# Optimization experiments

Hardware: AMD Instinct MI355X
Metric: run time of the kernel (lower is better)

## Reference

```python
import jax, jax.numpy as jnp
import numpy as np

N = 50000  # total nodes


def sage_conv(x, src, dst, Wl, Wr, b):
    # PyG SAGEConv with mean aggregation: out = mean_{j in N(i)} x_j @ Wl + x_i @ Wr + b
    agg = jax.ops.segment_sum(x[src], dst, num_segments=N)
    deg = jax.ops.segment_sum(jnp.ones((src.shape[0],), x.dtype), dst, num_segments=N)
    mean = agg / jnp.maximum(deg, 1.0)[:, None]
    return mean @ Wl + x @ Wr + b


def setup_inputs() -> dict:
    key = jax.random.key(0)
    ks = jax.random.split(key, 16)
    F_in, D, H, B, E1, E2, A = 128, 64, 128, 16, 800000, 200000, 2000
    s = lambda fan: 1.0 / np.sqrt(fan)
    return {
        "x": jax.random.normal(ks[0], (N, F_in), jnp.float32),
        "edge_index": jax.random.randint(ks[1], (2, E1), 0, N),
        "new_edges": jax.random.randint(ks[2], (B, 2, E2), 0, N),
        "target_nodes": jax.random.randint(ks[3], (B,), 0, N),
        "regions": jax.random.randint(ks[4], (B, A), 0, N),
        "W1l": jax.random.normal(ks[5], (F_in, D), jnp.float32) * s(F_in),
        "W1r": jax.random.normal(ks[6], (F_in, D), jnp.float32) * s(F_in),
        "b1": jnp.zeros((D,), jnp.float32),
        "W2l": jax.random.normal(ks[7], (D, D), jnp.float32) * s(D),
        "W2r": jax.random.normal(ks[8], (D, D), jnp.float32) * s(D),
        "b2": jnp.zeros((D,), jnp.float32),
        "Wm": jax.random.normal(ks[9], (D, H), jnp.float32) * s(D),
        "bm": jnp.zeros((H,), jnp.float32),
        "Wo": jax.random.normal(ks[10], (H, D), jnp.float32) * s(H),
        "bo": jnp.zeros((D,), jnp.float32),
    }


def reference(x, edge_index, new_edges, target_nodes, regions,
              W1l, W1r, b1, W2l, W2r, b2, Wm, bm, Wo, bo):
    # shared conv1 over base graph
    h1 = jax.nn.relu(sage_conv(x, edge_index[0], edge_index[1], W1l, W1r, b1))  # [N,D]

    def per_graph(edges, t, region):
        h2 = jax.nn.relu(sage_conv(h1, edges[0], edges[1], W2l, W2r, b2))  # [N,D]
        target_embed = h2[t]          # [D]
        region_embed = h2[region]     # [A,D]
        e = jax.nn.relu(region_embed @ Wm + bm)  # [A,H]
        r = e @ Wo + bo                           # [A,D]
        return r @ target_embed                   # [A]  (bilin_q)

    q = jax.vmap(per_graph)(new_edges, target_nodes, regions)  # [B,A]
    return q
```

## Files before the change

### kernel.cpp

```cpp
#include <hip/hip_runtime.h>
#include <hip/hip_bf16.h>

#define NN 50000
#define E1C 800000
#define E2C 200000
#define BC 16
#define AC 2000
#define FIN 128
#define DD 64
#define HH 128
#define SLOTS (AC + 1)
#define SCAP 64
#define SCAP2 32
#define NPART 8
#define PSZ (NN / NPART)
#define DEGB 2048
#define MARKB ((BC * SLOTS + 255) / 256)
#define GH1B ((NN + 3) / 4)
#define FILTB 196
#define Q_NBLK 32

__device__ __forceinline__ unsigned short f2bf(float f) {
  unsigned int u = __float_as_uint(f);
  unsigned int r = (u + 0x7FFFu + ((u >> 16) & 1u)) >> 16;
  return (unsigned short)r;
}
__device__ __forceinline__ float bf2f(unsigned short h) {
  return __uint_as_float((unsigned int)h << 16);
}

__global__ __launch_bounds__(256, 2) void k_lin1(const float* __restrict__ x,
    const float* __restrict__ W1l, const float* __restrict__ W1r,
    const float* __restrict__ b1,
    unsigned short* __restrict__ y, float* __restrict__ z) {
  __shared__ __align__(16) float Wsh[FIN][FIN];
  for (int i = threadIdx.x; i < FIN * FIN; i += 256) {
    int k = i >> 7, c = i & 127;
    Wsh[k][c] = (c < DD) ? W1l[k * DD + c] : W1r[k * DD + (c - DD)];
  }
  const int cg = threadIdx.x & 31, c0 = cg * 4;
  const int rg = threadIdx.x >> 5, r0 = rg * 4;
  float4 bias = make_float4(0.f, 0.f, 0.f, 0.f);
  if (cg >= 16) bias = *(const float4*)(b1 + c0 - DD);
  __syncthreads();
  const int ntiles = (NN + 31) / 32;
  for (int t = blockIdx.x; t < ntiles; t += gridDim.x) {
    int base = t * 32;
    int gr0 = base + r0;
    const float* xp0 = x + (size_t)min(gr0 + 0, NN - 1) * FIN;
    const float* xp1 = x + (size_t)min(gr0 + 1, NN - 1) * FIN;
    const float* xp2 = x + (size_t)min(gr0 + 2, NN - 1) * FIN;
    const float* xp3 = x + (size_t)min(gr0 + 3, NN - 1) * FIN;
    float acc[4][4] = {};
#pragma unroll 4
    for (int kk = 0; kk < FIN; kk += 4) {
      float4 xq0 = *(const float4*)(xp0 + kk);
      float4 xq1 = *(const float4*)(xp1 + kk);
      float4 xq2 = *(const float4*)(xp2 + kk);
      float4 xq3 = *(const float4*)(xp3 + kk);
#pragma unroll
      for (int j = 0; j < 4; ++j) {
        float4 wv = *(const float4*)&Wsh[kk + j][c0];
        float x0 = (j == 0) ? xq0.x : (j == 1) ? xq0.y : (j == 2) ? xq0.z : xq0.w;
        float x1 = (j == 0) ? xq1.x : (j == 1) ? xq1.y : (j == 2) ? xq1.z : xq1.w;
        float x2 = (j == 0) ? xq2.x : (j == 1) ? xq2.y : (j == 2) ? xq2.z : xq2.w;
        float x3 = (j == 0) ? xq3.x : (j == 1) ? xq3.y : (j == 2) ? xq3.z : xq3.w;
        acc[0][0] = fmaf(x0, wv.x, acc[0][0]); acc[0][1] = fmaf(x0, wv.y, acc[0][1]);
        acc[0][2] = fmaf(x0, wv.z, acc[0][2]); acc[0][3] = fmaf(x0, wv.w, acc[0][3]);
        acc[1][0] = fmaf(x1, wv.x, acc[1][0]); acc[1][1] = fmaf(x1, wv.y, acc[1][1]);
        acc[1][2] = fmaf(x1, wv.z, acc[1][2]); acc[1][3] = fmaf(x1, wv.w, acc[1][3]);
        acc[2][0] = fmaf(x2, wv.x, acc[2][0]); acc[2][1] = fmaf(x2, wv.y, acc[2][1]);
        acc[2][2] = fmaf(x2, wv.z, acc[2][2]); acc[2][3] = fmaf(x2, wv.w, acc[2][3]);
        acc[3][0] = fmaf(x3, wv.x, acc[3][0]); acc[3][1] = fmaf(x3, wv.y, acc[3][1]);
        acc[3][2] = fmaf(x3, wv.z, acc[3][2]); acc[3][3] = fmaf(x3, wv.w, acc[3][3]);
      }
    }
#pragma unroll
    for (int i = 0; i < 4; ++i) {
      int gr = base + r0 + i;
      if (gr < NN) {
        if (cg < 16) {
          ushort4 ob = make_ushort4(f2bf(acc[i][0]), f2bf(acc[i][1]),
                                    f2bf(acc[i][2]), f2bf(acc[i][3]));
          *(ushort4*)(y + (size_t)gr * DD + c0) = ob;
        } else {
          float4 o = make_float4(acc[i][0] + bias.x, acc[i][1] + bias.y,
                                 acc[i][2] + bias.z, acc[i][3] + bias.w);
          *(float4*)(z + (size_t)gr * DD + (c0 - DD)) = o;
        }
      }
    }
  }
}

__global__ __launch_bounds__(256) void k_prep(const int* __restrict__ src,
    const int* __restrict__ dst, int* __restrict__ degi, int* __restrict__ slots,
    const int* __restrict__ regions, const int* __restrict__ targets,
    int* __restrict__ mark, int* __restrict__ rep) {
  if (blockIdx.x < DEGB) {
    int part = blockIdx.x & (NPART - 1);
    int lb   = blockIdx.x >> 3;
    int nlb  = DEGB >> 3;
    int lo = part * PSZ, hi = lo + PSZ;
    for (int e = lb * 256 + threadIdx.x; e < E1C; e += nlb * 256) {
      int d = dst[e];
      if (d >= lo && d < hi) {
        int p = atomicAdd(&degi[d], 1);
        if (p < SCAP) slots[(size_t)d * SCAP + p] = src[e];
      }
    }
  } else {
    int i = (blockIdx.x - DEGB) * 256 + threadIdx.x;
    if (i >= BC * SLOTS) return;
    int b = i / SLOTS, k = i % SLOTS;
    int node = (k < AC) ? regions[b * AC + k] : targets[b];
    int old = atomicCAS(&mark[b * NN + node], -1, k);
    rep[i] = (old < 0) ? k : old;
  }
}

__global__ __launch_bounds__(256) void k_sparse2(const int* __restrict__ degi,
    const int* __restrict__ slots, const unsigned short* __restrict__ y,
    const float* __restrict__ z, float* __restrict__ h1,
    const int* __restrict__ ne, const int* __restrict__ mark,
    int* __restrict__ deg2i, int* __restrict__ slots2) {
  if (blockIdx.x < GH1B) {
    int w = blockIdx.x * 4 + (threadIdx.x >> 6);
    int lane = threadIdx.x & 63;
    if (w >= NN) return;
    int deg = degi[w];
    int n = min(deg, SCAP);
    const int* sp = slots + (size_t)w * SCAP;
    float acc = 0.f;
    int j = 0;
    for (; j + 4 <= n; j += 4) {
      int s0 = sp[j], s1 = sp[j + 1], s2 = sp[j + 2], s3 = sp[j + 3];
      float a0 = bf2f(y[(size_t)s0 * DD + lane]);
      float a1 = bf2f(y[(size_t)s1 * DD + lane]);
      float a2 = bf2f(y[(size_t)s2 * DD + lane]);
      float a3 = bf2f(y[(size_t)s3 * DD + lane]);
      acc += (a0 + a1) + (a2 + a3);
    }
    for (; j < n; ++j) acc += bf2f(y[(size_t)sp[j] * DD + lane]);
    float m = acc / fmaxf((float)deg, 1.f);
    h1[(size_t)w * DD + lane] = fmaxf(m + z[(size_t)w * DD + lane], 0.f);
  } else {
    int fid = blockIdx.x - GH1B;
    int b = fid / FILTB, eb = fid % FILTB;
    int e = eb * 1024 + threadIdx.x * 4;
    if (e >= E2C) return;
    const int* srcp = ne + (size_t)b * 2 * E2C;
    const int* dstp = srcp + E2C;
    int4 d4 = *(const int4*)(dstp + e);
    const int* mb = mark + (size_t)b * NN;
    int k0 = mb[d4.x], k1 = mb[d4.y], k2 = mb[d4.z], k3 = mb[d4.w];
    if (k0 >= 0) { int p = atomicAdd(&deg2i[b * SLOTS + k0], 1);
      if (p < SCAP2) slots2[((size_t)b * SLOTS + k0) * SCAP2 + p] = srcp[e]; }
    if (k1 >= 0) { int p = atomicAdd(&deg2i[b * SLOTS + k1], 1);
      if (p < SCAP2) slots2[((size_t)b * SLOTS + k1) * SCAP2 + p] = srcp[e + 1]; }
    if (k2 >= 0) { int p = atomicAdd(&deg2i[b * SLOTS + k2], 1);
      if (p < SCAP2) slots2[((size_t)b * SLOTS + k2) * SCAP2 + p] = srcp[e + 2]; }
    if (k3 >= 0) { int p = atomicAdd(&deg2i[b * SLOTS + k3], 1);
      if (p < SCAP2) slots2[((size_t)b * SLOTS + k3) * SCAP2 + p] = srcp[e + 3]; }
  }
}

__global__ __launch_bounds__(256, 4) void k_lin2(const float* __restrict__ h1,
    const float* __restrict__ W2l, const float* __restrict__ W2r,
    const float* __restrict__ b2,
    float* __restrict__ u, float* __restrict__ v) {
  __shared__ __align__(16) float Wsh[DD][128];
  for (int i = threadIdx.x; i < DD * 128; i += 256) {
    int k = i >> 7, c = i & 127;
    Wsh[k][c] = (c < DD) ? W2l[k * DD + c] : W2r[k * DD + (c - DD)];
  }
  const int cg = threadIdx.x & 31, c0 = cg * 4;
  const int rg = threadIdx.x >> 5, r0 = rg * 4;
  float4 bias = make_float4(0.f, 0.f, 0.f, 0.f);
  if (cg >= 16) bias = *(const float4*)(b2 + c0 - DD);
  __syncthreads();
  const int ntiles = (NN + 31) / 32;
  for (int t = blockIdx.x; t < ntiles; t += gridDim.x) {
    int base = t * 32;
    int gr0 = base + r0;
    const float* xp0 = h1 + (size_t)min(gr0 + 0, NN - 1) * DD;
    const float* xp1 = h1 + (size_t)min(gr0 + 1, NN - 1) * DD;
    const float* xp2 = h1 + (size_t)min(gr0 + 2, NN - 1) * DD;
    const float* xp3 = h1 + (size_t)min(gr0 + 3, NN - 1) * DD;
    float acc[4][4] = {};
#pragma unroll 4
    for (int kk = 0; kk < DD; kk += 4) {
      float4 xq0 = *(const float4*)(xp0 + kk);
      float4 xq1 = *(const float4*)(xp1 + kk);
      float4 xq2 = *(const float4*)(xp2 + kk);
      float4 xq3 = *(const float4*)(xp3 + kk);
#pragma unroll
      for (int j = 0; j < 4; ++j) {
        float4 wv = *(const float4*)&Wsh[kk + j][c0];
        float x0 = (j == 0) ? xq0.x : (j == 1) ? xq0.y : (j == 2) ? xq0.z : xq0.w;
        float x1 = (j == 0) ? xq1.x : (j == 1) ? xq1.y : (j == 2) ? xq1.z : xq1.w;
        float x2 = (j == 0) ? xq2.x : (j == 1) ? xq2.y : (j == 2) ? xq2.z : xq2.w;
        float x3 = (j == 0) ? xq3.x : (j == 1) ? xq3.y : (j == 2) ? xq3.z : xq3.w;
        acc[0][0] = fmaf(x0, wv.x, acc[0][0]); acc[0][1] = fmaf(x0, wv.y, acc[0][1]);
        acc[0][2] = fmaf(x0, wv.z, acc[0][2]); acc[0][3] = fmaf(x0, wv.w, acc[0][3]);
        acc[1][0] = fmaf(x1, wv.x, acc[1][0]); acc[1][1] = fmaf(x1, wv.y, acc[1][1]);
        acc[1][2] = fmaf(x1, wv.z, acc[1][2]); acc[1][3] = fmaf(x1, wv.w, acc[1][3]);
        acc[2][0] = fmaf(x2, wv.x, acc[2][0]); acc[2][1] = fmaf(x2, wv.y, acc[2][1]);
        acc[2][2] = fmaf(x2, wv.z, acc[2][2]); acc[2][3] = fmaf(x2, wv.w, acc[2][3]);
        acc[3][0] = fmaf(x3, wv.x, acc[3][0]); acc[3][1] = fmaf(x3, wv.y, acc[3][1]);
        acc[3][2] = fmaf(x3, wv.z, acc[3][2]); acc[3][3] = fmaf(x3, wv.w, acc[3][3]);
      }
    }
#pragma unroll
    for (int i = 0; i < 4; ++i) {
      int gr = base + r0 + i;
      if (gr < NN) {
        float4 o = make_float4(acc[i][0] + bias.x, acc[i][1] + bias.y,
                               acc[i][2] + bias.z, acc[i][3] + bias.w);
        if (cg < 16) *(float4*)(u + (size_t)gr * DD + c0) = o;
        else         *(float4*)(v + (size_t)gr * DD + (c0 - DD)) = o;
      }
    }
  }
}

__global__ __launch_bounds__(256) void k_gather_h2(const int* __restrict__ deg2i,
    const int* __restrict__ slots2, const int* __restrict__ rep,
    const int* __restrict__ regions, const int* __restrict__ targets,
    const float* __restrict__ u, const float* __restrict__ v,
    float* __restrict__ h2c) {
  int w = blockIdx.x * 4 + (threadIdx.x >> 6);
  int lane = threadIdx.x & 63;
  if (w >= BC * SLOTS) return;
  int b = w / SLOTS, k = w - b * SLOTS;
  int r = rep[w];
  int deg = deg2i[b * SLOTS + r];
  int n = min(deg, SCAP2);
  const int* sp = slots2 + ((size_t)b * SLOTS + r) * SCAP2;
  float acc = 0.f;
  int j = 0;
  for (; j + 4 <= n; j += 4) {
    int s0 = sp[j], s1 = sp[j + 1], s2 = sp[j + 2], s3 = sp[j + 3];
    float a0 = u[(size_t)s0 * DD + lane];
    float a1 = u[(size_t)s1 * DD + lane];
    float a2 = u[(size_t)s2 * DD + lane];
    float a3 = u[(size_t)s3 * DD + lane];
    acc += (a0 + a1) + (a2 + a3);
  }
  for (; j < n; ++j) acc += u[(size_t)sp[j] * DD + lane];
  int node = (k < AC) ? regions[b * AC + k] : targets[b];
  float m = acc / fmaxf((float)deg, 1.f);
  h2c[(size_t)w * DD + lane] = fmaxf(m + v[(size_t)node * DD + lane], 0.f);
}

__global__ __launch_bounds__(256) void k_q(const float* __restrict__ h2c,
    const float* __restrict__ Wm, const float* __restrict__ bm,
    const float* __restrict__ Wo, const float* __restrict__ bo,
    float* __restrict__ q) {
  __shared__ float W[DD][HH];
  __shared__ float bmL[HH], wtL[HH], te[DD];
  __shared__ float c0s;
  int b = blockIdx.y;
  for (int i = threadIdx.x; i < DD * HH; i += 256) W[i >> 7][i & 127] = Wm[i];
  if (threadIdx.x < HH) bmL[threadIdx.x] = bm[threadIdx.x];
  if (threadIdx.x < DD) te[threadIdx.x] = h2c[((size_t)b * SLOTS + AC) * DD + threadIdx.x];
  __syncthreads();
  if (threadIdx.x < HH) {
    float a = 0.f;
#pragma unroll
    for (int d = 0; d < DD; ++d) a = fmaf(Wo[threadIdx.x * DD + d], te[d], a);
    wtL[threadIdx.x] = a;
  } else if (threadIdx.x == HH) {
    float s = 0.f;
    for (int d = 0; d < DD; ++d) s += bo[d] * te[d];
    c0s = s;
  }
  __syncthreads();
  float cc = c0s;
  int lane = threadIdx.x & 63;
  int wv = threadIdx.x >> 6;
  int nwv = (blockDim.x >> 6) * gridDim.x;
  for (int a = blockIdx.x * 4 + wv; a < AC; a += nwv) {
    float hv = h2c[((size_t)b * SLOTS + a) * DD + lane];
    float a0 = 0.f, a1 = 0.f;
#pragma unroll
    for (int d = 0; d < DD; ++d) {
      float xd = __shfl(hv, d);
      a0 = fmaf(xd, W[d][lane], a0);
      a1 = fmaf(xd, W[d][lane + 64], a1);
    }
    float e0 = fmaxf(a0 + bmL[lane], 0.f);
    float e1 = fmaxf(a1 + bmL[lane + 64], 0.f);
    float p = fmaf(e0, wtL[lane], e1 * wtL[lane + 64]);
#pragma unroll
    for (int m = 32; m; m >>= 1) p += __shfl_xor(p, m);
    if (lane == 0) q[b * AC + a] = p + cc;
  }
}

extern "C" void kernel_launch(void* const* d_in, const int* in_sizes, int n_in,
                              void* d_out, int out_size, void* d_ws, size_t ws_size,
                              hipStream_t stream) {
  const float* x    = (const float*)d_in[0];
  const int*   ei   = (const int*)d_in[1];
  const int*   ne   = (const int*)d_in[2];
  const int*   tgt  = (const int*)d_in[3];
  const int*   reg  = (const int*)d_in[4];
  const float* W1l  = (const float*)d_in[5];
  const float* W1r  = (const float*)d_in[6];
  const float* b1   = (const float*)d_in[7];
  const float* W2l  = (const float*)d_in[8];
  const float* W2r  = (const float*)d_in[9];
  const float* b2   = (const float*)d_in[10];
  const float* Wm   = (const float*)d_in[11];
  const float* bm   = (const float*)d_in[12];
  const float* Wo   = (const float*)d_in[13];
  const float* bo   = (const float*)d_in[14];
  float* q = (float*)d_out;

  char* w = (char*)d_ws;
  size_t off = 0;
  auto alloc = [&](size_t bytes) { void* p = w + off; off = (off + bytes + 255) & ~(size_t)255; return p; };
  float* y_u   = (float*)alloc((size_t)NN * DD * 4);
  float* z_v   = (float*)alloc((size_t)NN * DD * 4);
  float* h1b   = (float*)alloc((size_t)NN * DD * 4);
  int*   degi  = (int*)alloc((size_t)NN * 4);
  int*   slots = (int*)alloc((size_t)NN * SCAP * 4);
  int*   mark  = (int*)alloc((size_t)BC * NN * 4);
  int*   rep   = (int*)alloc((size_t)BC * SLOTS * 4);
  int*   deg2i = (int*)alloc((size_t)BC * SLOTS * 4);
  int*   slots2= (int*)alloc((size_t)BC * SLOTS * SCAP2 * 4);
  float* h2c   = (float*)alloc((size_t)BC * SLOTS * DD * 4);
  unsigned short* y_bf = (unsigned short*)y_u;
  (void)ws_size; (void)n_in; (void)in_sizes; (void)out_size;

  hipMemsetAsync(degi,  0,    (size_t)NN * 4, stream);
  hipMemsetAsync(mark,  0xFF, (size_t)BC * NN * 4, stream);
  hipMemsetAsync(deg2i, 0,    (size_t)BC * SLOTS * 4, stream);

  const int* e_src = ei;
  const int* e_dst = ei + E1C;

  k_lin1<<<512, 256, 0, stream>>>(x, W1l, W1r, b1, y_bf, z_v);
  k_prep<<<DEGB + MARKB, 256, 0, stream>>>(e_src, e_dst, degi, slots, reg, tgt, mark, rep);
  k_sparse2<<<GH1B + BC * FILTB, 256, 0, stream>>>(degi, slots, y_bf, z_v, h1b,
                                                   ne, mark, deg2i, slots2);
  k_lin2<<<1024, 256, 0, stream>>>(h1b, W2l, W2r, b2, y_u, z_v);
  k_gather_h2<<<(BC * SLOTS + 3) / 4, 256, 0, stream>>>(deg2i, slots2, rep, reg, tgt,
                                                        y_u, z_v, h2c);
  k_q<<<dim3(Q_NBLK, BC), 256, 0, stream>>>(h2c, Wm, bm, Wo, bo, q);
}
```

Before: 310.1 us.

## Fuse layer-2 gather into q kernel, store neighbor projection in bf16, vectorize slot loads

Removes the separate k_gather_h2 kernel and its h2c buffer: the mean-aggregated layer-2 embedding is now computed in registers inside the q kernel, per region row and for the target row. The layer-2 neighbor projection u is written as bf16 instead of fp32, halving the bytes read by the gather. Slot index lists are read with int4 vector loads, and the layer-1 gather gains an 8-wide unrolled loop. This trades one kernel launch and a global round trip for lower bf16 precision on u. It also makes each of the 32×16 q blocks redo the target gather, and lengthens the per-wave critical path in k_q2.

New measurement: 314.7 us. No clear change (+1.5%).

```diff
diff --git a/kernel.cpp b/kernel.cpp
--- a/kernel.cpp
+++ b/kernel.cpp
@@ -133,12 +133,25 @@
     const int* sp = slots + (size_t)w * SCAP;
     float acc = 0.f;
     int j = 0;
+    for (; j + 8 <= n; j += 8) {
+      int4 sA = *(const int4*)(sp + j);
+      int4 sB = *(const int4*)(sp + j + 4);
+      float a0 = bf2f(y[(size_t)sA.x * DD + lane]);
+      float a1 = bf2f(y[(size_t)sA.y * DD + lane]);
+      float a2 = bf2f(y[(size_t)sA.z * DD + lane]);
+      float a3 = bf2f(y[(size_t)sA.w * DD + lane]);
+      float a4 = bf2f(y[(size_t)sB.x * DD + lane]);
+      float a5 = bf2f(y[(size_t)sB.y * DD + lane]);
+      float a6 = bf2f(y[(size_t)sB.z * DD + lane]);
+      float a7 = bf2f(y[(size_t)sB.w * DD + lane]);
+      acc += ((a0 + a1) + (a2 + a3)) + ((a4 + a5) + (a6 + a7));
+    }
     for (; j + 4 <= n; j += 4) {
-      int s0 = sp[j], s1 = sp[j + 1], s2 = sp[j + 2], s3 = sp[j + 3];
-      float a0 = bf2f(y[(size_t)s0 * DD + lane]);
-      float a1 = bf2f(y[(size_t)s1 * DD + lane]);
-      float a2 = bf2f(y[(size_t)s2 * DD + lane]);
-      float a3 = bf2f(y[(size_t)s3 * DD + lane]);
+      int4 sA = *(const int4*)(sp + j);
+      float a0 = bf2f(y[(size_t)sA.x * DD + lane]);
+      float a1 = bf2f(y[(size_t)sA.y * DD + lane]);
+      float a2 = bf2f(y[(size_t)sA.z * DD + lane]);
+      float a3 = bf2f(y[(size_t)sA.w * DD + lane]);
       acc += (a0 + a1) + (a2 + a3);
     }
     for (; j < n; ++j) acc += bf2f(y[(size_t)sp[j] * DD + lane]);
@@ -168,7 +181,7 @@
 __global__ __launch_bounds__(256, 4) void k_lin2(const float* __restrict__ h1,
     const float* __restrict__ W2l, const float* __restrict__ W2r,
     const float* __restrict__ b2,
-    float* __restrict__ u, float* __restrict__ v) {
+    unsigned short* __restrict__ u, float* __restrict__ v) {
   __shared__ __align__(16) float Wsh[DD][128];
   for (int i = threadIdx.x; i < DD * 128; i += 256) {
     int k = i >> 7, c = i & 127;
@@ -215,24 +228,23 @@
     for (int i = 0; i < 4; ++i) {
       int gr = base + r0 + i;
       if (gr < NN) {
-        float4 o = make_float4(acc[i][0] + bias.x, acc[i][1] + bias.y,
-                               acc[i][2] + bias.z, acc[i][3] + bias.w);
-        if (cg < 16) *(float4*)(u + (size_t)gr * DD + c0) = o;
-        else         *(float4*)(v + (size_t)gr * DD + (c0 - DD)) = o;
-      }
-    }
-  }
-}
-
-__global__ __launch_bounds__(256) void k_gather_h2(const int* __restrict__ deg2i,
-    const int* __restrict__ slots2, const int* __restrict__ rep,
-    const int* __restrict__ regions, const int* __restrict__ targets,
-    const float* __restrict__ u, const float* __restrict__ v,
-    float* __restrict__ h2c) {
-  int w = blockIdx.x * 4 + (threadIdx.x >> 6);
-  int lane = threadIdx.x & 63;
-  if (w >= BC * SLOTS) return;
-  int b = w / SLOTS, k = w - b * SLOTS;
+        if (cg < 16) {
+          ushort4 ob = make_ushort4(f2bf(acc[i][0]), f2bf(acc[i][1]),
+                                    f2bf(acc[i][2]), f2bf(acc[i][3]));
+          *(ushort4*)(u + (size_t)gr * DD + c0) = ob;
+        } else {
+          float4 o = make_float4(acc[i][0] + bias.x, acc[i][1] + bias.y,
+                                 acc[i][2] + bias.z, acc[i][3] + bias.w);
+          *(float4*)(v + (size_t)gr * DD + (c0 - DD)) = o;
+        }
+      }
+    }
+  }
+}
+
+__device__ __forceinline__ float gather_h2_reg(const int* deg2i, const int* slots2,
+    const int* rep, const unsigned short* u, const float* v,
+    int b, int w, int node, int lane) {
   int r = rep[w];
   int deg = deg2i[b * SLOTS + r];
   int n = min(deg, SCAP2);
@@ -240,20 +252,22 @@
   float acc = 0.f;
   int j = 0;
   for (; j + 4 <= n; j += 4) {
-    int s0 = sp[j], s1 = sp[j + 1], s2 = sp[j + 2], s3 = sp[j + 3];
-    float a0 = u[(size_t)s0 * DD + lane];
-    float a1 = u[(size_t)s1 * DD + lane];
-    float a2 = u[(size_t)s2 * DD + lane];
-    float a3 = u[(size_t)s3 * DD + lane];
+    int4 sA = *(const int4*)(sp + j);
+    float a0 = bf2f(u[(size_t)sA.x * DD + lane]);
+    float a1 = bf2f(u[(size_t)sA.y * DD + lane]);
+    float a2 = bf2f(u[(size_t)sA.z * DD + lane]);
+    float a3 = bf2f(u[(size_t)sA.w * DD + lane]);
     acc += (a0 + a1) + (a2 + a3);
   }
-  for (; j < n; ++j) acc += u[(size_t)sp[j] * DD + lane];
-  int node = (k < AC) ? regions[b * AC + k] : targets[b];
+  for (; j < n; ++j) acc += bf2f(u[(size_t)sp[j] * DD + lane]);
   float m = acc / fmaxf((float)deg, 1.f);
-  h2c[(size_t)w * DD + lane] = fmaxf(m + v[(size_t)node * DD + lane], 0.f);
-}
-
-__global__ __launch_bounds__(256) void k_q(const float* __restrict__ h2c,
+  return fmaxf(m + v[(size_t)node * DD + lane], 0.f);
+}
+
+__global__ __launch_bounds__(256) void k_q2(const int* __restrict__ deg2i,
+    const int* __restrict__ slots2, const int* __restrict__ rep,
+    const int* __restrict__ regions, const int* __restrict__ targets,
+    const unsigned short* __restrict__ u, const float* __restrict__ v,
     const float* __restrict__ Wm, const float* __restrict__ bm,
     const float* __restrict__ Wo, const float* __restrict__ bo,
     float* __restrict__ q) {
@@ -263,7 +277,11 @@
   int b = blockIdx.y;
   for (int i = threadIdx.x; i < DD * HH; i += 256) W[i >> 7][i & 127] = Wm[i];
   if (threadIdx.x < HH) bmL[threadIdx.x] = bm[threadIdx.x];
-  if (threadIdx.x < DD) te[threadIdx.x] = h2c[((size_t)b * SLOTS + AC) * DD + threadIdx.x];
+  if (threadIdx.x < DD) {
+    int tn = targets[b];
+    te[threadIdx.x] = gather_h2_reg(deg2i, slots2, rep, u, v,
+                                    b, b * SLOTS + AC, tn, threadIdx.x);
+  }
   __syncthreads();
   if (threadIdx.x < HH) {
     float a = 0.f;
@@ -281,7 +299,8 @@
   int wv = threadIdx.x >> 6;
   int nwv = (blockDim.x >> 6) * gridDim.x;
   for (int a = blockIdx.x * 4 + wv; a < AC; a += nwv) {
-    float hv = h2c[((size_t)b * SLOTS + a) * DD + lane];
+    int node = regions[b * AC + a];
+    float hv = gather_h2_reg(deg2i, slots2, rep, u, v, b, b * SLOTS + a, node, lane);
     float a0 = 0.f, a1 = 0.f;
 #pragma unroll
     for (int d = 0; d < DD; ++d) {
@@ -330,7 +349,6 @@
   int*   rep   = (int*)alloc((size_t)BC * SLOTS * 4);
   int*   deg2i = (int*)alloc((size_t)BC * SLOTS * 4);
   int*   slots2= (int*)alloc((size_t)BC * SLOTS * SCAP2 * 4);
-  float* h2c   = (float*)alloc((size_t)BC * SLOTS * DD * 4);
   unsigned short* y_bf = (unsigned short*)y_u;
   (void)ws_size; (void)n_in; (void)in_sizes; (void)out_size;
 
@@ -345,8 +363,7 @@
   k_prep<<<DEGB + MARKB, 256, 0, stream>>>(e_src, e_dst, degi, slots, reg, tgt, mark, rep);
   k_sparse2<<<GH1B + BC * FILTB, 256, 0, stream>>>(degi, slots, y_bf, z_v, h1b,
                                                    ne, mark, deg2i, slots2);
-  k_lin2<<<1024, 256, 0, stream>>>(h1b, W2l, W2r, b2, y_u, z_v);
-  k_gather_h2<<<(BC * SLOTS + 3) / 4, 256, 0, stream>>>(deg2i, slots2, rep, reg, tgt,
-                                                        y_u, z_v, h2c);
-  k_q<<<dim3(Q_NBLK, BC), 256, 0, stream>>>(h2c, Wm, bm, Wo, bo, q);
-}
+  k_lin2<<<1024, 256, 0, stream>>>(h1b, W2l, W2r, b2, y_bf, z_v);
+  k_q2<<<dim3(Q_NBLK, BC), 256, 0, stream>>>(deg2i, slots2, rep, reg, tgt,
+                                             y_bf, z_v, Wm, bm, Wo, bo, q);
+}
```
